# Kernel tuning notes

Measured on AMD Instinct MI355X. Metric: run time of the kernel, lower is better.

The kernel has to match this reference:

```python
import jax, jax.numpy as jnp
import numpy as np

NUM_HEADS = 32
MICRO_BATCHES = 2
TOP_K = 2
LN_EPS = 1e-5


def _mha(x, scale, bias, wq, wk, wv, wo):
    # Pre-LN multi-head self-attention with residual (RealSelfAttention).
    B, S, D = x.shape
    H = NUM_HEADS
    hd = D // H
    res = x
    mu = jnp.mean(x, axis=-1, keepdims=True)
    xc = x - mu
    var = jnp.mean(xc * xc, axis=-1, keepdims=True)
    xn = xc / jnp.sqrt(var + LN_EPS) * scale + bias
    q = (xn @ wq.T).reshape(B, S, H, hd).transpose(0, 2, 1, 3)
    k = (xn @ wk.T).reshape(B, S, H, hd).transpose(0, 2, 1, 3)
    v = (xn @ wv.T).reshape(B, S, H, hd).transpose(0, 2, 1, 3)
    scores = jnp.einsum('bhqd,bhkd->bhqk', q, k) * (1.0 / np.sqrt(hd).astype(np.float32))
    attn = jax.nn.softmax(scores, axis=-1)
    o = jnp.einsum('bhqk,bhkd->bhqd', attn, v).transpose(0, 2, 1, 3).reshape(B, S, D)
    return o @ wo.T + res


def setup_inputs() -> dict:
    key = jax.random.key(0)
    D, E, F = 1024, 8, 4096
    B, S = 4, 1024
    ks = jax.random.split(key, 16)
    w = lambda k, shape: (jax.random.normal(k, shape, dtype=jnp.float32) * 0.02)
    return {
        'x': jax.random.normal(ks[0], (B, S, D), dtype=jnp.float32),
        'ln1_scale': jnp.ones((D,), jnp.float32),
        'ln1_bias': jnp.zeros((D,), jnp.float32),
        'wq1': w(ks[1], (D, D)), 'wk1': w(ks[2], (D, D)),
        'wv1': w(ks[3], (D, D)), 'wo1': w(ks[4], (D, D)),
        'gate_w': w(ks[5], (E, D)),
        'exp_w1': w(ks[6], (E, F, D)), 'exp_b1': jnp.zeros((E, F), jnp.float32),
        'exp_w2': w(ks[7], (E, D, F)), 'exp_b2': jnp.zeros((E, D), jnp.float32),
        'ln2_scale': jnp.ones((D,), jnp.float32),
        'ln2_bias': jnp.zeros((D,), jnp.float32),
        'wq2': w(ks[8], (D, D)), 'wk2': w(ks[9], (D, D)),
        'wv2': w(ks[10], (D, D)), 'wo2': w(ks[11], (D, D)),
    }


def reference(x, ln1_scale, ln1_bias, wq1, wk1, wv1, wo1, gate_w,
              exp_w1, exp_b1, exp_w2, exp_b2,
              ln2_scale, ln2_bias, wq2, wk2, wv2, wo2):
    B, S, D = x.shape
    E = exp_w1.shape[0]
    # PreOps: attention layer L (per-sample, so full-batch apply == per-microbatch apply)
    y = _mha(x, ln1_scale, ln1_bias, wq1, wk1, wv1, wo1)
    # Gate: logits + top-k indices computed in source but never applied to tokens.
    flat = y.reshape(B * S, D)
    logits = flat @ gate_w.T
    _ = jax.lax.top_k(logits, TOP_K)  # indices unused downstream (faithful to source)
    # Dispatch (all_to_all on 1 device == identity): per-microbatch flat tokens are
    # chunked equally across local experts.
    T = (B // MICRO_BATCHES) * S            # tokens per microbatch
    toks = y.reshape(MICRO_BATCHES, E, T // E, D)
    h = jax.nn.gelu(jnp.einsum('metd,efd->metf', toks, exp_w1) + exp_b1[None, :, None, :],
                    approximate=False)
    eo = jnp.einsum('metf,edf->metd', h, exp_w2) + exp_b2[None, :, None, :]
    # Combine (identity) + PostOps: attention layer L+1
    z = eo.reshape(B, S, D)
    out = _mha(z, ln2_scale, ln2_bias, wq2, wk2, wv2, wo2)
    return out
```

## Files before the change

kernel.cpp:

```cpp
#include <hip/hip_runtime.h>
#include <hip/hip_bf16.h>

typedef __attribute__((ext_vector_type(8))) short bf16x8;
typedef __attribute__((ext_vector_type(4))) float f32x4;
typedef __attribute__((ext_vector_type(4))) short short4v;

#define DEV __device__ __forceinline__

DEV short f2bf(float f) {
  union { float f; unsigned u; } x; x.f = f;
  unsigned r = x.u + 0x7fffu + ((x.u >> 16) & 1u);
  return (short)(r >> 16);
}

DEV short f2bf_hw(float f) {
  union { __hip_bfloat16 h; short s; } c;
  c.h = __float2bfloat16(f);
  return c.s;
}

DEV bf16x8 cvt8(f32x4 a, f32x4 b) {
  union { short s[8]; bf16x8 v; } o;
  o.s[0] = f2bf_hw(a[0]); o.s[1] = f2bf_hw(a[1]);
  o.s[2] = f2bf_hw(a[2]); o.s[3] = f2bf_hw(a[3]);
  o.s[4] = f2bf_hw(b[0]); o.s[5] = f2bf_hw(b[1]);
  o.s[6] = f2bf_hw(b[2]); o.s[7] = f2bf_hw(b[3]);
  return o.v;
}

template <int N> DEV void vmwait() {
  if constexpr (N == 0) asm volatile("s_waitcnt vmcnt(0)" ::: "memory");
  else if constexpr (N == 3) asm volatile("s_waitcnt vmcnt(3)" ::: "memory");
  else if constexpr (N == 4) asm volatile("s_waitcnt vmcnt(4)" ::: "memory");
  else if constexpr (N == 6) asm volatile("s_waitcnt vmcnt(6)" ::: "memory");
}

#define GL2LDS16(g, l) __builtin_amdgcn_global_load_lds(                      \
    (const __attribute__((address_space(1))) void*)(g),                       \
    (__attribute__((address_space(3))) void*)(l), 16, 0, 0)

__global__ __launch_bounds__(256) void k_cast_bf16(const float* __restrict__ s,
                                                   short* __restrict__ d, int n4) {
  int i = blockIdx.x * 256 + threadIdx.x;
  if (i >= n4) return;
  float4 v = ((const float4*)s)[i];
  short4v o;
  o[0] = f2bf(v.x); o[1] = f2bf(v.y); o[2] = f2bf(v.z); o[3] = f2bf(v.w);
  ((short4v*)d)[i] = o;
}

__global__ __launch_bounds__(256)
void k_ln(const float* __restrict__ X, const float* __restrict__ G,
          const float* __restrict__ Bi, short* __restrict__ Y) {
  const int row = blockIdx.x, t = threadIdx.x;
  const float4 v = ((const float4*)(X + (size_t)row * 1024))[t];
  float s = v.x + v.y + v.z + v.w;
  float s2 = v.x * v.x + v.y * v.y + v.z * v.z + v.w * v.w;
#pragma unroll
  for (int m = 1; m < 64; m <<= 1) { s += __shfl_xor(s, m); s2 += __shfl_xor(s2, m); }
  __shared__ float rs[4], rq[4];
  const int w = t >> 6, lane = t & 63;
  if (lane == 0) { rs[w] = s; rq[w] = s2; }
  __syncthreads();
  s = rs[0] + rs[1] + rs[2] + rs[3];
  s2 = rq[0] + rq[1] + rq[2] + rq[3];
  const float mu = s * (1.f / 1024.f);
  const float var = s2 * (1.f / 1024.f) - mu * mu;
  const float rstd = rsqrtf(var + 1e-5f);
  const float4 g = ((const float4*)G)[t];
  const float4 bi = ((const float4*)Bi)[t];
  short4v o;
  o[0] = f2bf((v.x - mu) * rstd * g.x + bi.x);
  o[1] = f2bf((v.y - mu) * rstd * g.y + bi.y);
  o[2] = f2bf((v.z - mu) * rstd * g.z + bi.z);
  o[3] = f2bf((v.w - mu) * rstd * g.w + bi.w);
  ((short4v*)(Y + (size_t)row * 1024))[t] = o;
}

template <int EPI, int EXPERT, int BN, int BF32>
__global__ __launch_bounds__(256)
void k_gemm_bt(const short* __restrict__ A, const void* __restrict__ Btv,
               void* __restrict__ Cv, const float* __restrict__ Res,
               const float* __restrict__ Bias, int M, int N, int K, int xt) {
  constexpr int NF = BN / 32;
  constexpr int BR = BN / 64;
  constexpr int LOADS = 2 + (BF32 ? NF : BR);
  __shared__ __attribute__((aligned(16))) short As[3][128 * 32];
  __shared__ __attribute__((aligned(16))) char Braw[3][BN * 32 * (BF32 ? 4 : 2)];
  const int tid = threadIdx.x;
  const int w = tid >> 6, lane = tid & 63;
  const int r16 = lane & 15, kg = lane >> 4;
  const int wr = w >> 1, wc = w & 1;

  const int bid = blockIdx.x;
  int bx;
  size_t rowBase, bOff = 0, biasOff = 0;
  if constexpr (EXPERT) {
    int e = bid & 7, mb = (bid >> 3) & 1, by = (bid >> 4) & 1;
    bx = bid >> 5;
    rowBase = (size_t)by * 128 + (size_t)(mb * 8 + e) * 256;
    bOff = (size_t)e * N * K;
    biasOff = (size_t)e * N;
  } else {
    int y7 = bid & 7, r = bid >> 3;
    bx = r % xt;
    rowBase = (size_t)(y7 + 8 * (r / xt)) * 128;
  }
  const size_t col0 = (size_t)bx * BN;
  const short* Ab = A + rowBase * K;
  const short* Bb16 = (const short*)Btv + bOff + col0 * K;
  const float* Bb32 = (const float*)Btv + bOff + col0 * K;

  f32x4 acc[4][NF] = {};

  auto stage = [&](int buf, int k0) {
#pragma unroll
    for (int i = 0; i < 2; ++i) {
      int c = (i * 4 + w) * 64 + lane;
      int row = c >> 2;
      int sl = (c & 3) ^ (row & 3);
      GL2LDS16(Ab + (size_t)row * K + k0 + sl * 8, (char*)As[buf] + (size_t)(i * 4 + w) * 1024);
    }
    if constexpr (BF32) {
#pragma unroll
      for (int i = 0; i < NF; ++i) {
        int c = i * 256 + tid;
        int row = c >> 3;
        int sl = (c & 7) ^ (row & 7);
        GL2LDS16(Bb32 + (size_t)row * K + k0 + sl * 4, (char*)Braw[buf] + (size_t)(i * 4 + w) * 1024);
      }
    } else {
#pragma unroll
      for (int i = 0; i < BR; ++i) {
        int c = i * 256 + tid;
        int row = c >> 2;
        int sl = (c & 3) ^ (row & 3);
        GL2LDS16(Bb16 + (size_t)row * K + k0 + sl * 8, (char*)Braw[buf] + (size_t)(i * 4 + w) * 1024);
      }
    }
  };

  stage(0, 0);
  stage(1, 32);
  vmwait<LOADS>();
  __builtin_amdgcn_s_barrier();

  int cur = 0;
  for (int k0 = 0; k0 < K; k0 += 32) {
    int cn = cur + 1; if (cn == 3) cn = 0;
    int c2 = cn + 1; if (c2 == 3) c2 = 0;
    const bool more = (k0 + 64 < K);
    if (more) stage(c2, k0 + 64);

    bf16x8 af[4], bg[NF];
#pragma unroll
    for (int m = 0; m < 4; ++m) {
      int row = wr * 64 + m * 16 + r16;
      af[m] = *(const bf16x8*)(As[cur] + row * 32 + (kg ^ (row & 3)) * 8);
    }
    if constexpr (BF32) {
      const float* Bf = (const float*)Braw[cur];
#pragma unroll
      for (int n = 0; n < NF; ++n) {
        int row = wc * (BN / 2) + n * 16 + r16;
        int s0 = (2 * kg) ^ (row & 7), s1 = (2 * kg + 1) ^ (row & 7);
        f32x4 fa = *(const f32x4*)(Bf + row * 32 + s0 * 4);
        f32x4 fb = *(const f32x4*)(Bf + row * 32 + s1 * 4);
        bg[n] = cvt8(fa, fb);
      }
    } else {
      const short* Bh = (const short*)Braw[cur];
#pragma unroll
      for (int n = 0; n < NF; ++n) {
        int row = wc * (BN / 2) + n * 16 + r16;
        bg[n] = *(const bf16x8*)(Bh + row * 32 + (kg ^ (row & 3)) * 8);
      }
    }
#pragma unroll
    for (int m = 0; m < 4; ++m)
#pragma unroll
      for (int n = 0; n < NF; ++n)
        acc[m][n] = __builtin_amdgcn_mfma_f32_16x16x32_bf16(af[m], bg[n], acc[m][n], 0, 0, 0);

    if (more) vmwait<LOADS>(); else vmwait<0>();
    __builtin_amdgcn_s_barrier();
    cur = cn;
  }

#pragma unroll
  for (int m = 0; m < 4; ++m) {
    size_t grow0 = rowBase + wr * 64 + m * 16 + kg * 4;
#pragma unroll
    for (int n = 0; n < NF; ++n) {
      size_t gcol = col0 + wc * (BN / 2) + n * 16 + r16;
#pragma unroll
      for (int r = 0; r < 4; ++r) {
        size_t idx = (grow0 + r) * (size_t)N + gcol;
        float v = acc[m][n][r];
        if constexpr (EPI == 1 || EPI == 4) v += Res[idx];
        if constexpr (EPI == 2 || EPI == 3) v += Bias[biasOff + gcol];
        if constexpr (EPI == 2) v = 0.5f * v * (1.f + erff(v * 0.70710678118654752f));
        if constexpr (EPI <= 2) ((short*)Cv)[idx] = f2bf(v);
        else                    ((float*)Cv)[idx] = v;
      }
    }
  }
  (void)M;
}

__global__ __launch_bounds__(256, 3)
void k_attn(const short* __restrict__ QKV, short* __restrict__ O) {
  const int bid = blockIdx.x;
  const int qt = bid >> 7, h = bid & 31, b = (bid >> 5) & 3;
  const int tid = threadIdx.x, w = tid >> 6, lane = tid & 63;
  const int r16 = lane & 15, kg = lane >> 4;

  __shared__ __attribute__((aligned(16))) short Kl[2][128 * 32];
  __shared__ __attribute__((aligned(16))) short Vt[2][32 * 128];
  __shared__ __attribute__((aligned(16))) short Pl[4][16 * 128];

  const size_t tb = (size_t)b * 1024;
  const int qbase = qt * 128 + w * 32;

  bf16x8 aq[2];
#pragma unroll
  for (int f = 0; f < 2; ++f)
    aq[f] = *(const bf16x8*)(QKV + (tb + qbase + f * 16 + r16) * 3072 + h * 32 + kg * 8);

  f32x4 acc[2][2] = {};
  float lreg[2][4] = {};
  const float scale = 0.17677669529663687f;

  auto stageK = [&](int bid2, int kc) {
#pragma unroll
    for (int i = 0; i < 2; ++i) {
      int c = (i * 4 + w) * 64 + lane;
      int row = c >> 2;
      int sl = (c & 3) ^ (row & 3);
      GL2LDS16(QKV + (tb + kc * 128 + row) * 3072 + 1024 + h * 32 + sl * 8,
               (char*)Kl[bid2] + (size_t)(i * 4 + w) * 1024);
    }
  };

  stageK(0, 0);
  {
    int c0 = tid,        vr0 = c0 >> 2, d00 = (c0 & 3) * 8;
    int c1 = 256 + tid,  vr1 = c1 >> 2, d01 = (c1 & 3) * 8;
    bf16x8 v0 = *(const bf16x8*)(QKV + (tb + vr0) * 3072 + 2048 + h * 32 + d00);
    bf16x8 v1 = *(const bf16x8*)(QKV + (tb + vr1) * 3072 + 2048 + h * 32 + d01);
#pragma unroll
    for (int j = 0; j < 8; ++j) {
      int da = d00 + j, db = d01 + j;
      Vt[0][((da * 128 + vr0) ^ ((da & 7) << 3))] = v0[j];
      Vt[0][((db * 128 + vr1) ^ ((db & 7) << 3))] = v1[j];
    }
  }
  __syncthreads();

  int bi = 0;
  for (int kc = 0; kc < 8; ++kc) {
    bf16x8 nv0, nv1;
    int nvr0 = 0, nd0 = 0, nvr1 = 0, nd1 = 0;
    if (kc < 7) {
      stageK(bi ^ 1, kc + 1);
      const short* Vg = QKV + (tb + (size_t)(kc + 1) * 128) * 3072 + 2048 + h * 32;
      int c0 = tid;       nvr0 = c0 >> 2; nd0 = (c0 & 3) * 8;
      int c1 = 256 + tid; nvr1 = c1 >> 2; nd1 = (c1 & 3) * 8;
      nv0 = *(const bf16x8*)(Vg + (size_t)nvr0 * 3072 + nd0);
      nv1 = *(const bf16x8*)(Vg + (size_t)nvr1 * 3072 + nd1);
    }

    f32x4 s[2][8];
#pragma unroll
    for (int kt = 0; kt < 8; ++kt) {
      int row = kt * 16 + r16;
      bf16x8 bk = *(const bf16x8*)(Kl[bi] + row * 32 + (kg ^ (row & 3)) * 8);
      f32x4 zz = {0.f, 0.f, 0.f, 0.f};
      s[0][kt] = __builtin_amdgcn_mfma_f32_16x16x32_bf16(aq[0], bk, zz, 0, 0, 0);
      s[1][kt] = __builtin_amdgcn_mfma_f32_16x16x32_bf16(aq[1], bk, zz, 0, 0, 0);
    }

#pragma unroll
    for (int f = 0; f < 2; ++f)
#pragma unroll
      for (int r = 0; r < 4; ++r) {
        float sum = 0.f;
#pragma unroll
        for (int kt = 0; kt < 8; ++kt) {
          float p = __expf(s[f][kt][r] * scale);
          s[f][kt][r] = p;
          sum += p;
        }
#pragma unroll
        for (int m = 1; m < 16; m <<= 1) sum += __shfl_xor(sum, m);
        lreg[f][r] += sum;
      }

    short* P = Pl[w];
#pragma unroll
    for (int f = 0; f < 2; ++f) {
#pragma unroll
      for (int kt = 0; kt < 8; ++kt)
#pragma unroll
        for (int r = 0; r < 4; ++r) {
          int row = kg * 4 + r;
          P[((row * 128 + kt * 16 + r16) ^ ((row & 7) << 3))] = f2bf(s[f][kt][r]);
        }
#pragma unroll
      for (int ks = 0; ks < 4; ++ks) {
        bf16x8 pa = *(const bf16x8*)(P + ((r16 * 128 + ks * 32 + kg * 8) ^ ((r16 & 7) << 3)));
#pragma unroll
        for (int dt = 0; dt < 2; ++dt) {
          int vrow = dt * 16 + r16;
          bf16x8 bv = *(const bf16x8*)(Vt[bi] + ((vrow * 128 + ks * 32 + kg * 8) ^ ((vrow & 7) << 3)));
          acc[f][dt] = __builtin_amdgcn_mfma_f32_16x16x32_bf16(pa, bv, acc[f][dt], 0, 0, 0);
        }
      }
    }

    if (kc < 7) {
#pragma unroll
      for (int j = 0; j < 8; ++j) {
        int da = nd0 + j, db = nd1 + j;
        Vt[bi ^ 1][((da * 128 + nvr0) ^ ((da & 7) << 3))] = nv0[j];
        Vt[bi ^ 1][((db * 128 + nvr1) ^ ((db & 7) << 3))] = nv1[j];
      }
    }

    __syncthreads();
    bi ^= 1;
  }

#pragma unroll
  for (int f = 0; f < 2; ++f)
#pragma unroll
    for (int r = 0; r < 4; ++r) {
      float inv = 1.f / lreg[f][r];
      size_t qrow = tb + qbase + f * 16 + kg * 4 + r;
#pragma unroll
      for (int dt = 0; dt < 2; ++dt)
        O[qrow * 1024 + h * 32 + dt * 16 + r16] = f2bf(acc[f][dt][r] * inv);
    }
}

extern "C" void kernel_launch(void* const* d_in, const int* in_sizes, int n_in,
                              void* d_out, int out_size, void* d_ws, size_t ws_size,
                              hipStream_t stream) {
  const float* x    = (const float*)d_in[0];
  const float* ln1s = (const float*)d_in[1];
  const float* ln1b = (const float*)d_in[2];
  const float* wq1  = (const float*)d_in[3];
  const float* wk1  = (const float*)d_in[4];
  const float* wv1  = (const float*)d_in[5];
  const float* wo1  = (const float*)d_in[6];
  const float* ew1  = (const float*)d_in[8];
  const float* eb1  = (const float*)d_in[9];
  const float* ew2  = (const float*)d_in[10];
  const float* eb2  = (const float*)d_in[11];
  const float* ln2s = (const float*)d_in[12];
  const float* ln2b = (const float*)d_in[13];
  const float* wq2  = (const float*)d_in[14];
  const float* wk2  = (const float*)d_in[15];
  const float* wv2  = (const float*)d_in[16];
  const float* wo2  = (const float*)d_in[17];

  char* ws = (char*)d_ws;
  size_t off = 0;
  auto alloc = [&](size_t bytes) {
    char* p = ws + off;
    off += (bytes + 255) & ~(size_t)255;
    return p;
  };
  short* wqkv1b = (short*)alloc(3072ull * 1024 * 2);
  short* wo1b   = (short*)alloc(1024ull * 1024 * 2);
  short* wqkv2b = (short*)alloc(3072ull * 1024 * 2);
  short* wo2b   = (short*)alloc(1024ull * 1024 * 2);
  short* xnb    = (short*)alloc(4096ull * 1024 * 2);
  short* qkvo   = (short*)alloc(4096ull * 4096 * 2);
  short* ybf    = (short*)alloc(4096ull * 1024 * 2);
  float* zf     = (float*)alloc(4096ull * 1024 * 4);
  (void)ws_size; (void)in_sizes; (void)n_in; (void)out_size;

  short* QKV = qkvo;
  short* Ob  = qkvo + 4096ull * 3072;
  short* hb  = qkvo;

  auto cast = [&](const float* s, short* d, size_t n) {
    int n4 = (int)(n / 4);
    k_cast_bf16<<<(n4 + 255) / 256, 256, 0, stream>>>(s, d, n4);
  };
  cast(wq1, wqkv1b,           1048576);
  cast(wk1, wqkv1b + 1048576, 1048576);
  cast(wv1, wqkv1b + 2097152, 1048576);
  cast(wo1, wo1b,             1048576);
  cast(wq2, wqkv2b,           1048576);
  cast(wk2, wqkv2b + 1048576, 1048576);
  cast(wv2, wqkv2b + 2097152, 1048576);
  cast(wo2, wo2b,             1048576);

  k_ln<<<4096, 256, 0, stream>>>(x, ln1s, ln1b, xnb);
  k_gemm_bt<0, 0, 128, 0><<<768, 256, 0, stream>>>(xnb, wqkv1b, QKV, nullptr, nullptr, 4096, 3072, 1024, 24);
  k_attn<<<1024, 256, 0, stream>>>(QKV, Ob);
  k_gemm_bt<1, 0, 64, 0><<<512, 256, 0, stream>>>(Ob, wo1b, ybf, x, nullptr, 4096, 1024, 1024, 16);
  k_gemm_bt<2, 1, 128, 1><<<1024, 256, 0, stream>>>(ybf, ew1, hb, nullptr, eb1, 256, 4096, 1024, 0);
  k_gemm_bt<3, 1, 64, 1><<<512, 256, 0, stream>>>(hb, ew2, zf, nullptr, eb2, 256, 1024, 4096, 0);
  k_ln<<<4096, 256, 0, stream>>>(zf, ln2s, ln2b, xnb);
  k_gemm_bt<0, 0, 128, 0><<<768, 256, 0, stream>>>(xnb, wqkv2b, QKV, nullptr, nullptr, 4096, 3072, 1024, 24);
  k_attn<<<1024, 256, 0, stream>>>(QKV, Ob);
  k_gemm_bt<4, 0, 64, 0><<<512, 256, 0, stream>>>(Ob, wo2b, (float*)d_out, zf, nullptr, 4096, 1024, 1024, 16);
}
```

Before: 541.1 us.

## Split attention over two KV halves with a separate normalize-and-combine kernel

The attention kernel now splits each (query tile, head, batch) block into two blocks. Each block handles half of the key/value chunks and writes its unnormalized fp32 output and its row sums to workspace. A new finalize kernel adds the two partials, divides by the combined row sum and writes bf16. The goal is to double the block count so the attention grid fills the GPU better and has a smaller tail. The cost is an extra launch and extra fp32 traffic through workspace. The bf16 conversion helper in cvt8 also switches from the HIP intrinsic to the manual rounding routine.

```diff
diff --git a/kernel.cpp b/kernel.cpp
--- a/kernel.cpp
+++ b/kernel.cpp
@@ -1,5 +1,4 @@
 #include <hip/hip_runtime.h>
-#include <hip/hip_bf16.h>
 
 typedef __attribute__((ext_vector_type(8))) short bf16x8;
 typedef __attribute__((ext_vector_type(4))) float f32x4;
@@ -13,18 +12,12 @@
   return (short)(r >> 16);
 }
 
-DEV short f2bf_hw(float f) {
-  union { __hip_bfloat16 h; short s; } c;
-  c.h = __float2bfloat16(f);
-  return c.s;
-}
-
 DEV bf16x8 cvt8(f32x4 a, f32x4 b) {
   union { short s[8]; bf16x8 v; } o;
-  o.s[0] = f2bf_hw(a[0]); o.s[1] = f2bf_hw(a[1]);
-  o.s[2] = f2bf_hw(a[2]); o.s[3] = f2bf_hw(a[3]);
-  o.s[4] = f2bf_hw(b[0]); o.s[5] = f2bf_hw(b[1]);
-  o.s[6] = f2bf_hw(b[2]); o.s[7] = f2bf_hw(b[3]);
+  o.s[0] = f2bf(a[0]); o.s[1] = f2bf(a[1]);
+  o.s[2] = f2bf(a[2]); o.s[3] = f2bf(a[3]);
+  o.s[4] = f2bf(b[0]); o.s[5] = f2bf(b[1]);
+  o.s[6] = f2bf(b[2]); o.s[7] = f2bf(b[3]);
   return o.v;
 }
 
@@ -209,9 +202,11 @@
 }
 
 __global__ __launch_bounds__(256, 3)
-void k_attn(const short* __restrict__ QKV, short* __restrict__ O) {
+void k_attn(const short* __restrict__ QKV, float* __restrict__ On,
+            float* __restrict__ Lw) {
   const int bid = blockIdx.x;
-  const int qt = bid >> 7, h = bid & 31, b = (bid >> 5) & 3;
+  const int half = bid >> 10, low = bid & 1023;
+  const int qt = low >> 7, h = low & 31, b = (low >> 5) & 3;
   const int tid = threadIdx.x, w = tid >> 6, lane = tid & 63;
   const int r16 = lane & 15, kg = lane >> 4;
 
@@ -221,6 +216,7 @@
 
   const size_t tb = (size_t)b * 1024;
   const int qbase = qt * 128 + w * 32;
+  const int kc0 = half * 4;
 
   bf16x8 aq[2];
 #pragma unroll
@@ -242,12 +238,13 @@
     }
   };
 
-  stageK(0, 0);
+  stageK(0, kc0);
   {
     int c0 = tid,        vr0 = c0 >> 2, d00 = (c0 & 3) * 8;
     int c1 = 256 + tid,  vr1 = c1 >> 2, d01 = (c1 & 3) * 8;
-    bf16x8 v0 = *(const bf16x8*)(QKV + (tb + vr0) * 3072 + 2048 + h * 32 + d00);
-    bf16x8 v1 = *(const bf16x8*)(QKV + (tb + vr1) * 3072 + 2048 + h * 32 + d01);
+    const short* Vg = QKV + (tb + (size_t)kc0 * 128) * 3072 + 2048 + h * 32;
+    bf16x8 v0 = *(const bf16x8*)(Vg + (size_t)vr0 * 3072 + d00);
+    bf16x8 v1 = *(const bf16x8*)(Vg + (size_t)vr1 * 3072 + d01);
 #pragma unroll
     for (int j = 0; j < 8; ++j) {
       int da = d00 + j, db = d01 + j;
@@ -258,10 +255,11 @@
   __syncthreads();
 
   int bi = 0;
-  for (int kc = 0; kc < 8; ++kc) {
+  for (int it = 0; it < 4; ++it) {
+    const int kc = kc0 + it;
     bf16x8 nv0, nv1;
     int nvr0 = 0, nd0 = 0, nvr1 = 0, nd1 = 0;
-    if (kc < 7) {
+    if (it < 3) {
       stageK(bi ^ 1, kc + 1);
       const short* Vg = QKV + (tb + (size_t)(kc + 1) * 128) * 3072 + 2048 + h * 32;
       int c0 = tid;       nvr0 = c0 >> 2; nd0 = (c0 & 3) * 8;
@@ -318,7 +316,7 @@
       }
     }
 
-    if (kc < 7) {
+    if (it < 3) {
 #pragma unroll
       for (int j = 0; j < 8; ++j) {
         int da = nd0 + j, db = nd1 + j;
@@ -331,16 +329,35 @@
     bi ^= 1;
   }
 
+  float* Oh = On + ((size_t)half << 22);
 #pragma unroll
   for (int f = 0; f < 2; ++f)
 #pragma unroll
     for (int r = 0; r < 4; ++r) {
-      float inv = 1.f / lreg[f][r];
       size_t qrow = tb + qbase + f * 16 + kg * 4 + r;
 #pragma unroll
       for (int dt = 0; dt < 2; ++dt)
-        O[qrow * 1024 + h * 32 + dt * 16 + r16] = f2bf(acc[f][dt][r] * inv);
-    }
+        Oh[qrow * 1024 + h * 32 + dt * 16 + r16] = acc[f][dt][r];
+      if (r16 == 0)
+        Lw[(size_t)half * 131072 + qrow * 32 + h] = lreg[f][r];
+    }
+}
+
+__global__ __launch_bounds__(256)
+void k_attn_fin(const float* __restrict__ On, const float* __restrict__ Lw,
+                short* __restrict__ O) {
+  const int r = blockIdx.x, t = threadIdx.x;
+  const int c = t * 4, h = c >> 5;
+  const size_t i0 = (size_t)r * 1024 + c;
+  float4 n0 = *(const float4*)(On + i0);
+  float4 n1 = *(const float4*)(On + (1ull << 22) + i0);
+  float inv = 1.f / (Lw[(size_t)r * 32 + h] + Lw[131072 + (size_t)r * 32 + h]);
+  short4v o;
+  o[0] = f2bf((n0.x + n1.x) * inv);
+  o[1] = f2bf((n0.y + n1.y) * inv);
+  o[2] = f2bf((n0.z + n1.z) * inv);
+  o[3] = f2bf((n0.w + n1.w) * inv);
+  *(short4v*)(O + i0) = o;
 }
 
 extern "C" void kernel_launch(void* const* d_in, const int* in_sizes, int n_in,
@@ -379,6 +396,8 @@
   short* qkvo   = (short*)alloc(4096ull * 4096 * 2);
   short* ybf    = (short*)alloc(4096ull * 1024 * 2);
   float* zf     = (float*)alloc(4096ull * 1024 * 4);
+  float* onum   = (float*)alloc(2ull * 4096 * 1024 * 4);
+  float* lw     = (float*)alloc(2ull * 131072 * 4);
   (void)ws_size; (void)in_sizes; (void)n_in; (void)out_size;
 
   short* QKV = qkvo;
@@ -400,12 +419,14 @@
 
   k_ln<<<4096, 256, 0, stream>>>(x, ln1s, ln1b, xnb);
   k_gemm_bt<0, 0, 128, 0><<<768, 256, 0, stream>>>(xnb, wqkv1b, QKV, nullptr, nullptr, 4096, 3072, 1024, 24);
-  k_attn<<<1024, 256, 0, stream>>>(QKV, Ob);
+  k_attn<<<2048, 256, 0, stream>>>(QKV, onum, lw);
+  k_attn_fin<<<4096, 256, 0, stream>>>(onum, lw, Ob);
   k_gemm_bt<1, 0, 64, 0><<<512, 256, 0, stream>>>(Ob, wo1b, ybf, x, nullptr, 4096, 1024, 1024, 16);
   k_gemm_bt<2, 1, 128, 1><<<1024, 256, 0, stream>>>(ybf, ew1, hb, nullptr, eb1, 256, 4096, 1024, 0);
   k_gemm_bt<3, 1, 64, 1><<<512, 256, 0, stream>>>(hb, ew2, zf, nullptr, eb2, 256, 1024, 4096, 0);
   k_ln<<<4096, 256, 0, stream>>>(zf, ln2s, ln2b, xnb);
   k_gemm_bt<0, 0, 128, 0><<<768, 256, 0, stream>>>(xnb, wqkv2b, QKV, nullptr, nullptr, 4096, 3072, 1024, 24);
-  k_attn<<<1024, 256, 0, stream>>>(QKV, Ob);
+  k_attn<<<2048, 256, 0, stream>>>(QKV, onum, lw);
+  k_attn_fin<<<4096, 256, 0, stream>>>(onum, lw, Ob);
   k_gemm_bt<4, 0, 64, 0><<<512, 256, 0, stream>>>(Ob, wo2b, (float*)d_out, zf, nullptr, 4096, 1024, 1024, 16);
 }
```

Measured after the change: 568.2 us. +5.0%, slower.
